# Kernel tuning notes

Hardware: AMD Instinct MI355X
Metric: run time of the kernel (lower is better)

The kernel has to match this reference:

```python
import jax, jax.numpy as jnp
import numpy as np

B = 64; L = 1024; M = 3; PATCH = 16; STRIDE = 8
LEN_S = (L - PATCH) // STRIDE + 2   # patch_num incl. extra patch from replication pad (=128)
LEN_P = 12                           # tokenized prompt length
T = LEN_S + LEN_P                    # total tokens fed to GPT2 (=140)
D = 768; NH = 12; HD = D // NH       # GPT2-small dims
NL = 6; DMLP = 3072                  # gpt_layers, GPT2 MLP width
DFF = 768; NCLS = 10; DLC = 128      # d_ff hidden slice, classes, d_l_comp
SEQ = np.array([1] * LEN_S + [2] * LEN_P)

def _pe(n, d):
    pos = np.arange(n)[:, None].astype(np.float64)
    i = np.arange(0, d, 2)[None, :].astype(np.float64)
    ang = pos / np.power(10000.0, i / d)
    pe = np.zeros((n, d), np.float32)
    pe[:, 0::2] = np.sin(ang); pe[:, 1::2] = np.cos(ang)
    return pe

PE = jnp.asarray(_pe(LEN_S, D))
# allocation matrix (T x 2), column-normalized: maps 2 coarse nodes back to fine tokens
_afc = np.zeros((T, 2), np.float32)
_afc[:LEN_S, 0] = 1.0 / LEN_S; _afc[LEN_S:, 1] = 1.0 / LEN_P
AFC = jnp.asarray(_afc)

def _build_edges():
    # bidirectional chain edges over the token sequence; edge-type 1 = both endpoints are patch tokens
    e, m = [], []
    for i in range(T - 1):
        t = 1 if (SEQ[i] == 1 and SEQ[i + 1] == 1) else 0
        e += [(i, i + 1), (i + 1, i)]; m += [t, t]
    e = np.array(e, np.int32).T            # (2, E0)
    E0 = e.shape[1]
    off = np.arange(B, dtype=np.int32) * T # expand_edges: per-sample node offsets
    ee = (e[:, None, :] + off[None, :, None]).reshape(2, -1)
    mm = np.tile(np.array(m, np.int32), B)
    seg = np.repeat(np.arange(B, dtype=np.int32), E0) * 2 + mm  # (graph, edge-type) segment id
    return ee, seg

def layer_norm(x, g, b, eps=1e-5):
    mu = x.mean(-1, keepdims=True)
    v = ((x - mu) ** 2).mean(-1, keepdims=True)
    return (x - mu) * jax.lax.rsqrt(v + eps) * g + b

def _fwd(x_enc, conv_w, prompt_emb, wpe, ln1_g, ln1_b, attn_w, attn_b, proj_w, proj_b,
         ln2_g, ln2_b, fc1_w, fc1_b, fc2_w, fc2_b, lnf_g, lnf_b,
         ll1_w, ll1_b, ll0_w, ll0_b, l2s_w, l2s_b, w_l2s,
         lnp_g, lnp_b, out_w, out_b, edge_index, edge_seg):
    Bb = x_enc.shape[0]
    # ---- patching (ReplicationPad1d + unfold + 'b m n p -> b n (p m)') ----
    xt = jnp.transpose(x_enc, (0, 2, 1))                                   # (B,M,L)
    xt = jnp.concatenate([xt, jnp.repeat(xt[:, :, -1:], STRIDE, axis=-1)], axis=-1)
    idx = np.arange(LEN_S)[:, None] * STRIDE + np.arange(PATCH)[None, :]
    patches = xt[:, :, idx]                                                # (B,M,N,P)
    inp = jnp.transpose(patches, (0, 2, 3, 1)).reshape(Bb, LEN_S, PATCH * M)
    # ---- DataEmbedding: circular conv1d token embedding + sinusoid pos ----
    xc = jnp.transpose(inp, (0, 2, 1))
    xc = jnp.concatenate([xc[:, :, -1:], xc, xc[:, :, :1]], axis=-1)       # circular pad k=3
    val = jax.lax.conv_general_dilated(xc, conv_w, (1,), 'VALID',
                                       dimension_numbers=('NCH', 'OIH', 'NCH'))
    enc = jnp.transpose(val, (0, 2, 1)) + PE                               # (B,LEN_S,D)
    h0 = jnp.concatenate([enc, jnp.broadcast_to(prompt_emb, (Bb, LEN_P, D))], axis=1)
    # ---- edge weights: cosine similarity + per-(graph,edge-type) softmax norm ----
    src, dst = edge_index[0], edge_index[1]
    flat = h0.reshape(Bb * T, D)
    fs, fd = flat[src], flat[dst]
    cos = jnp.sum(fs * fd, -1) / (jnp.linalg.norm(fs, axis=-1) * jnp.linalg.norm(fd, axis=-1) + 1e-8)
    nseg = 2 * Bb
    mx = jax.ops.segment_max(cos, edge_seg, num_segments=nseg)
    ex = jnp.exp(cos - mx[edge_seg])
    ew = ex / (jax.ops.segment_sum(ex, edge_seg, num_segments=nseg)[edge_seg] + 1e-8)
    # ---- coarse (large) node embeddings via large_layer1/0 on detached features ----
    o1 = jax.lax.stop_gradient(h0[:, :LEN_S]).reshape(Bb, LEN_S * D)
    o2 = jax.lax.stop_gradient(h0[:, LEN_S:]).reshape(Bb, LEN_P * D)
    l_h = jnp.stack([o1 @ ll1_w + ll1_b, o2 @ ll0_w + ll0_b], axis=1)      # (B,2,D)
    # ---- GPT2-with-GNN blocks ----
    h = h0 + wpe[:T]
    causal = np.tril(np.ones((T, T), dtype=bool))
    scale = 1.0 / np.sqrt(HD)
    for l in range(NL):
        x = layer_norm(h, ln1_g[l], ln1_b[l])
        qkv = x @ attn_w[l] + attn_b[l]
        q, k, v = [t.reshape(Bb, T, NH, HD) for t in jnp.split(qkv, 3, axis=-1)]
        s = jnp.einsum('bqhd,bkhd->bhqk', q, k) * scale
        s = jnp.where(causal, s, jnp.finfo(s.dtype).min)
        a = jax.nn.softmax(s, axis=-1)
        o = jnp.einsum('bhqk,bkhd->bqhd', a, v).reshape(Bb, T, D)
        h = h + o @ proj_w[l] + proj_b[l]
        # edge-weighted message passing fused after attention (irregular gather/scatter)
        hf = h.reshape(Bb * T, D)
        agg = jax.ops.segment_sum(ew[:, None] * hf[src], dst, num_segments=Bb * T)
        h = h + agg.reshape(Bb, T, D)
        # MLP (GPT2 gelu_new ~ tanh approx)
        x2 = layer_norm(h, ln2_g[l], ln2_b[l])
        h = h + (jax.nn.gelu(x2 @ fc1_w[l] + fc1_b[l], approximate=True) @ fc2_w[l] + fc2_b[l])
        # coarse 2-node complete graph message passing + large->small fusion via afc/l2s
        l_h = l_h + l_h[:, ::-1, :]
        h = h + w_l2s * jnp.einsum('tl,bld->btd', AFC, l_h[:, :, :DLC] @ l2s_w + l2s_b)
    h = layer_norm(h, lnf_g, lnf_b)
    # ---- classification head: slice d_ff, gelu, flatten, layernorm, linear ----
    z = jax.nn.gelu(h[:, :, :DFF], approximate=False).reshape(Bb, -1)
    z = layer_norm(z, lnp_g, lnp_b)
    return z @ out_w + out_b

def setup_inputs():
    key = jax.random.key(0)
    ks = iter(jax.random.split(key, 40))
    r = lambda *s: jax.random.normal(next(ks), s, jnp.float32) * 0.02
    ee, seg = _build_edges()
    return dict(
        x_enc=jax.random.normal(next(ks), (B, L, M), jnp.float32),
        x_mark_enc=jax.random.normal(next(ks), (B, L, 4), jnp.float32),
        conv_w=r(D, PATCH * M, 3),
        prompt_emb=r(1, LEN_P, D),
        wpe=r(1024, D),
        ln1_g=jnp.ones((NL, D)), ln1_b=jnp.zeros((NL, D)),
        attn_w=r(NL, D, 3 * D), attn_b=jnp.zeros((NL, 3 * D)),
        proj_w=r(NL, D, D), proj_b=jnp.zeros((NL, D)),
        ln2_g=jnp.ones((NL, D)), ln2_b=jnp.zeros((NL, D)),
        fc1_w=r(NL, D, DMLP), fc1_b=jnp.zeros((NL, DMLP)),
        fc2_w=r(NL, DMLP, D), fc2_b=jnp.zeros((NL, D)),
        lnf_g=jnp.ones((D,)), lnf_b=jnp.zeros((D,)),
        ll1_w=r(LEN_S * D, D), ll1_b=jnp.zeros((D,)),
        ll0_w=r(LEN_P * D, D), ll0_b=jnp.zeros((D,)),
        l2s_w=r(DLC, D), l2s_b=jnp.zeros((D,)),
        w_l2s=jnp.float32(0.5),
        lnp_g=jnp.ones((DFF * T,)), lnp_b=jnp.zeros((DFF * T,)),
        out_w=r(DFF * T, NCLS), out_b=jnp.zeros((NCLS,)),
        edge_index=jnp.asarray(ee), edge_seg=jnp.asarray(seg),
    )

def reference(x_enc, x_mark_enc, conv_w, prompt_emb, wpe, ln1_g, ln1_b, attn_w, attn_b,
              proj_w, proj_b, ln2_g, ln2_b, fc1_w, fc1_b, fc2_w, fc2_b, lnf_g, lnf_b,
              ll1_w, ll1_b, ll0_w, ll0_b, l2s_w, l2s_b, w_l2s, lnp_g, lnp_b,
              out_w, out_b, edge_index, edge_seg):
    # x_mark_enc is accepted (matching the torch forward signature) but unused
    return _fwd(x_enc, conv_w, prompt_emb, wpe, ln1_g, ln1_b, attn_w, attn_b, proj_w, proj_b,
                ln2_g, ln2_b, fc1_w, fc1_b, fc2_w, fc2_b, lnf_g, lnf_b,
                ll1_w, ll1_b, ll0_w, ll0_b, l2s_w, l2s_b, w_l2s,
                lnp_g, lnp_b, out_w, out_b, edge_index, edge_seg)
```

## Files before the change

kernel.cpp:

```cpp
#include <hip/hip_runtime.h>
#include <math.h>

#define Bz     64
#define LENS   128
#define LENP   12
#define Tz     140
#define Dz     768
#define NHz    12
#define HDz    64
#define NLz    6
#define DMLPz  3072
#define NCLSz  10
#define EPBz   278
#define NTOKz  (Bz*Tz)
#define ZDIMz  (Tz*Dz)
#define KBIGz  (LENS*Dz)
#define KSMALLz (LENP*Dz)
#define PSTR   168

typedef float f32x4 __attribute__((ext_vector_type(4)));
typedef unsigned int u32x4 __attribute__((ext_vector_type(4)));
typedef short short8 __attribute__((ext_vector_type(8)));

__device__ __forceinline__ float wave_sum(float v){
  #pragma unroll
  for (int m = 32; m; m >>= 1) v += __shfl_xor(v, m);
  return v;
}
__device__ __forceinline__ float wave_max(float v){
  #pragma unroll
  for (int m = 32; m; m >>= 1) v = fmaxf(v, __shfl_xor(v, m));
  return v;
}
__device__ __forceinline__ float red16_max(float v){
  v = fmaxf(v, __shfl_xor(v, 1));
  v = fmaxf(v, __shfl_xor(v, 2));
  v = fmaxf(v, __shfl_xor(v, 4));
  v = fmaxf(v, __shfl_xor(v, 8));
  return v;
}
__device__ __forceinline__ float red16_sum(float v){
  v += __shfl_xor(v, 1); v += __shfl_xor(v, 2);
  v += __shfl_xor(v, 4); v += __shfl_xor(v, 8);
  return v;
}
__device__ __forceinline__ float gelu_tanh(float u){
  float c = 0.7978845608028654f * (u + 0.044715f * u * u * u);
  return 0.5f * u * (1.0f + tanhf(c));
}
__device__ __forceinline__ float gelu_exact(float u){
  return 0.5f * u * (1.0f + erff(u * 0.7071067811865476f));
}

__device__ __forceinline__ unsigned int f2bf(float x){
  unsigned int u = __float_as_uint(x);
  return (u + 0x7fffu + ((u >> 16) & 1u)) >> 16;
}
__device__ __forceinline__ float bf2f(unsigned int h){
  return __uint_as_float(h << 16);
}

__device__ __forceinline__ f32x4 mfma_bf16(u32x4 a, u32x4 b, f32x4 c){
  asm("v_mfma_f32_16x16x32_bf16 %0, %1, %2, %0" : "+v"(c) : "v"(a), "v"(b));
  return c;
}

__device__ __forceinline__ short8 pun(u32x4 u){
  union { u32x4 u; short8 s; } x; x.u = u; return x.s;
}
__device__ __forceinline__ f32x4 mfma_b(u32x4 a, u32x4 b, f32x4 c){
  return __builtin_amdgcn_mfma_f32_16x16x32_bf16(pun(a), pun(b), c, 0, 0, 0);
}

__device__ __forceinline__ void cvt_hilo(f32x4 x0, f32x4 x1, u32x4& h, u32x4& l){
  unsigned int h0 = f2bf(x0[0]), h1 = f2bf(x0[1]), h2 = f2bf(x0[2]), h3 = f2bf(x0[3]);
  unsigned int h4 = f2bf(x1[0]), h5 = f2bf(x1[1]), h6 = f2bf(x1[2]), h7 = f2bf(x1[3]);
  unsigned int l0 = f2bf(x0[0] - bf2f(h0)), l1 = f2bf(x0[1] - bf2f(h1));
  unsigned int l2 = f2bf(x0[2] - bf2f(h2)), l3 = f2bf(x0[3] - bf2f(h3));
  unsigned int l4 = f2bf(x1[0] - bf2f(h4)), l5 = f2bf(x1[1] - bf2f(h5));
  unsigned int l6 = f2bf(x1[2] - bf2f(h6)), l7 = f2bf(x1[3] - bf2f(h7));
  h[0] = h0 | (h1 << 16); h[1] = h2 | (h3 << 16);
  h[2] = h4 | (h5 << 16); h[3] = h6 | (h7 << 16);
  l[0] = l0 | (l1 << 16); l[1] = l2 | (l3 << 16);
  l[2] = l4 | (l5 << 16); l[3] = l6 | (l7 << 16);
}

__global__ void k_pe(float* pe){
  int idx = blockIdx.x * 256 + threadIdx.x;
  int s = idx / Dz, o = idx % Dz;
  int ie = o & ~1;
  double ang = (double)s * pow(10000.0, -(double)ie / (double)Dz);
  pe[idx] = (o & 1) ? (float)cos(ang) : (float)sin(ang);
}

__global__ void k_cwt(const float* __restrict__ cw, float* __restrict__ cwt){
  int idx = blockIdx.x * 256 + threadIdx.x;
  int o = idx % Dz, j = idx / Dz;
  int i = j % 48, k = j / 48;
  cwt[j * Dz + o] = cw[o * 144 + i * 3 + k];
}

__global__ __launch_bounds__(256) void k_conv(const float* __restrict__ x_enc,
                                              const float* __restrict__ cwt,
                                              const float* __restrict__ pe,
                                              float* __restrict__ h0){
  int b = blockIdx.x / LENS, s = blockIdx.x % LENS;
  int tid = threadIdx.x;
  __shared__ float in144[144];
  if (tid < 144){
    int k = tid / 48, i = tid % 48;
    int sp = (s + k - 1 + LENS) % LENS;
    int p = i / 3, m = i % 3;
    int j = sp * 8 + p; if (j > 1023) j = 1023;
    in144[tid] = x_enc[(b * 1024 + j) * 3 + m];
  }
  __syncthreads();
  for (int o = tid; o < Dz; o += 256){
    float acc = pe[s * Dz + o];
    #pragma unroll 8
    for (int j = 0; j < 144; ++j) acc += in144[j] * cwt[j * Dz + o];
    h0[((size_t)(b * Tz + s)) * Dz + o] = acc;
  }
}

__global__ void k_prompt(const float* __restrict__ pr, float* __restrict__ h0){
  int idx = blockIdx.x * 256 + threadIdx.x;
  int b = idx / (LENP * Dz), r = idx % (LENP * Dz);
  h0[((size_t)(b * Tz + LENS)) * Dz + r] = pr[r];
}

__global__ void k_norms(const float* __restrict__ h0, float* __restrict__ nrm){
  int n = blockIdx.x, lane = threadIdx.x;
  const float* r = h0 + (size_t)n * Dz;
  float s = 0.f;
  for (int d = lane; d < Dz; d += 64){ float v = r[d]; s += v * v; }
  s = wave_sum(s);
  if (lane == 0) nrm[n] = sqrtf(s);
}

__global__ void k_ecos(const float* __restrict__ h0, const int* __restrict__ eidx,
                       const float* __restrict__ nrm, float* __restrict__ cosb){
  int e = blockIdx.x, lane = threadIdx.x;
  int sN = eidx[e], dN = eidx[Bz * EPBz + e];
  const float* a = h0 + (size_t)sN * Dz;
  const float* b = h0 + (size_t)dN * Dz;
  float s = 0.f;
  for (int d = lane; d < Dz; d += 64) s += a[d] * b[d];
  s = wave_sum(s);
  if (lane == 0) cosb[e] = s / (nrm[sN] * nrm[dN] + 1e-8f);
}

__global__ __launch_bounds__(256) void k_esoft(const float* __restrict__ cosb,
                                               const int* __restrict__ eseg,
                                               float* __restrict__ ew){
  int b = blockIdx.x, tid = threadIdx.x;
  __shared__ float c[EPBz];
  __shared__ unsigned char gg[EPBz];
  __shared__ float r0[256], r1[256];
  for (int e = tid; e < EPBz; e += 256){
    c[e] = cosb[b * EPBz + e];
    gg[e] = (unsigned char)(eseg[b * EPBz + e] - 2 * b);
  }
  __syncthreads();
  float m0 = -1e30f, m1 = -1e30f;
  for (int e = tid; e < EPBz; e += 256){
    if (gg[e]) m1 = fmaxf(m1, c[e]); else m0 = fmaxf(m0, c[e]);
  }
  r0[tid] = m0; r1[tid] = m1; __syncthreads();
  for (int s = 128; s; s >>= 1){
    if (tid < s){ r0[tid] = fmaxf(r0[tid], r0[tid+s]); r1[tid] = fmaxf(r1[tid], r1[tid+s]); }
    __syncthreads();
  }
  m0 = r0[0]; m1 = r1[0]; __syncthreads();
  float s0 = 0.f, s1 = 0.f;
  for (int e = tid; e < EPBz; e += 256){
    float ex = expf(c[e] - (gg[e] ? m1 : m0));
    c[e] = ex;
    if (gg[e]) s1 += ex; else s0 += ex;
  }
  r0[tid] = s0; r1[tid] = s1; __syncthreads();
  for (int s = 128; s; s >>= 1){
    if (tid < s){ r0[tid] += r0[tid+s]; r1[tid] += r1[tid+s]; }
    __syncthreads();
  }
  s0 = r0[0]; s1 = r1[0];
  for (int e = tid; e < EPBz; e += 256)
    ew[b * EPBz + e] = c[e] / ((gg[e] ? s1 : s0) + 1e-8f);
}

__global__ void k_fills(const float* __restrict__ b1, const float* __restrict__ b0,
                        float* __restrict__ sbuf){
  int idx = blockIdx.x * 256 + threadIdx.x;
  int d = idx % Dz;
  sbuf[idx] = b1[d] + b0[d];
}

__global__ __launch_bounds__(256) void k_splitk(const float* __restrict__ Abase, int aOff,
                                                const float* __restrict__ W,
                                                float* __restrict__ Cacc,
                                                int K, int kChunk){
  __shared__ __align__(16) float As[16 * 65];
  __shared__ __align__(16) float Ws[16 * 64];
  int tid = threadIdx.x, tx = tid % 16, ty = tid / 16;
  int n0 = blockIdx.x * 64;
  int kb = blockIdx.y * kChunk;
  int ke = kb + kChunk; if (ke > K) ke = K;
  float acc[16];
  #pragma unroll
  for (int i = 0; i < 16; ++i) acc[i] = 0.f;
  for (int kk = kb; kk < ke; kk += 16){
    #pragma unroll
    for (int r = 0; r < 4; ++r){
      int idx = tid + r * 256; int k = idx & 15, m = idx >> 4;
      As[k * 65 + m] = Abase[(size_t)m * ZDIMz + aOff + kk + k];
    }
    #pragma unroll
    for (int r = 0; r < 4; ++r){
      int idx = tid + r * 256; int n = idx & 63, k = idx >> 6;
      Ws[k * 64 + n] = W[(size_t)(kk + k) * Dz + n0 + n];
    }
    __syncthreads();
    #pragma unroll
    for (int k = 0; k < 16; ++k){
      float a[4], bvv[4];
      #pragma unroll
      for (int i = 0; i < 4; ++i) a[i] = As[k * 65 + ty * 4 + i];
      #pragma unroll
      for (int j = 0; j < 4; ++j) bvv[j] = Ws[k * 64 + tx * 4 + j];
      #pragma unroll
      for (int i = 0; i < 4; ++i)
        #pragma unroll
        for (int j = 0; j < 4; ++j) acc[i * 4 + j] += a[i] * bvv[j];
    }
    __syncthreads();
  }
  #pragma unroll
  for (int i = 0; i < 4; ++i)
    #pragma unroll
    for (int j = 0; j < 4; ++j)
      atomicAdd(&Cacc[(size_t)(ty * 4 + i) * Dz + n0 + tx * 4 + j], acc[i * 4 + j]);
}

__global__ void k_psmall(const float* __restrict__ sbuf, const float* __restrict__ l2sw,
                         float* __restrict__ P){
  int idx = blockIdx.x * 256 + threadIdx.x;
  int b = idx / Dz, d = idx % Dz;
  float acc = 0.f;
  #pragma unroll 8
  for (int c = 0; c < 128; ++c) acc += sbuf[b * Dz + c] * l2sw[c * Dz + d];
  P[idx] = acc;
}

__global__ void k_addwpe(const float* __restrict__ h0, const float* __restrict__ wpe,
                         float* __restrict__ h){
  size_t idx = (size_t)blockIdx.x * 256 + threadIdx.x;
  int n = (int)(idx / Dz), d = (int)(idx % Dz);
  int t = n % Tz;
  h[idx] = h0[idx] + wpe[t * Dz + d];
}

__global__ __launch_bounds__(256) void k_ln(const float* __restrict__ in, float* __restrict__ out,
                                            const float* __restrict__ g, const float* __restrict__ bb){
  int row = blockIdx.x, tid = threadIdx.x;
  const float* r = in + (size_t)row * Dz;
  float v0 = r[tid], v1 = r[tid + 256], v2 = r[tid + 512];
  __shared__ float red[256];
  red[tid] = v0 + v1 + v2; __syncthreads();
  for (int s = 128; s; s >>= 1){ if (tid < s) red[tid] += red[tid + s]; __syncthreads(); }
  float mu = red[0] * (1.0f / Dz); __syncthreads();
  float d0 = v0 - mu, d1 = v1 - mu, d2 = v2 - mu;
  red[tid] = d0 * d0 + d1 * d1 + d2 * d2; __syncthreads();
  for (int s = 128; s; s >>= 1){ if (tid < s) red[tid] += red[tid + s]; __syncthreads(); }
  float rstd = rsqrtf(red[0] * (1.0f / Dz) + 1e-5f);
  float* o = out + (size_t)row * Dz;
  o[tid]       = d0 * rstd * g[tid]       + bb[tid];
  o[tid + 256] = d1 * rstd * g[tid + 256] + bb[tid + 256];
  o[tid + 512] = d2 * rstd * g[tid + 512] + bb[tid + 512];
}

__global__ __launch_bounds__(256) void k_wt(const float* __restrict__ W,
                                            unsigned short* __restrict__ WT,
                                            int K, int N){
  __shared__ float T[64][65];
  int k0 = blockIdx.y * 64, n0v = blockIdx.x * 64;
  int tid = threadIdx.x;
  int tx = tid & 15, ty = tid >> 4;
  #pragma unroll
  for (int rr = 0; rr < 4; ++rr){
    int row = rr * 16 + ty;
    const float* src = &W[(size_t)(k0 + row) * N + n0v + tx * 4];
    f32x4 v = *(const f32x4*)src;
    T[row][tx * 4]     = v[0];
    T[row][tx * 4 + 1] = v[1];
    T[row][tx * 4 + 2] = v[2];
    T[row][tx * 4 + 3] = v[3];
  }
  __syncthreads();
  #pragma unroll
  for (int s = 0; s < 2; ++s){
    int gi = tid + s * 256;
    int n = gi >> 3, kg = gi & 7;
    unsigned int h[8], l[8];
    #pragma unroll
    for (int j = 0; j < 8; ++j){
      float x = T[kg * 8 + j][n];
      h[j] = f2bf(x);
      l[j] = f2bf(x - bf2f(h[j]));
    }
    u32x4 hv, lv;
    hv[0] = h[0] | (h[1] << 16); hv[1] = h[2] | (h[3] << 16);
    hv[2] = h[4] | (h[5] << 16); hv[3] = h[6] | (h[7] << 16);
    lv[0] = l[0] | (l[1] << 16); lv[1] = l[2] | (l[3] << 16);
    lv[2] = l[4] | (l[5] << 16); lv[3] = l[6] | (l[7] << 16);
    size_t base = (size_t)(n0v + n) * 2 * K + (size_t)(k0 / 8 + kg) * 16;
    *(u32x4*)&WT[base]     = hv;
    *(u32x4*)&WT[base + 8] = lv;
  }
}

template<int MODE>
__global__ __launch_bounds__(256, 2) void k_bgemm(const float* __restrict__ A,
                                                  const unsigned short* __restrict__ WT,
                                                  const float* __restrict__ bias,
                                                  const float* __restrict__ R,
                                                  float* __restrict__ C, int M, int N, int K,
                                                  const float* __restrict__ P,
                                                  const float* __restrict__ l2sb,
                                                  const float* __restrict__ wl2s, float lscale){
  __shared__ __align__(16) unsigned short As[128 * 64];
  __shared__ __align__(16) unsigned short Bs[128 * 64];
  int tid = threadIdx.x;
  int n0 = blockIdx.x * 128, m0 = blockIdx.y * 128;
  int w = tid >> 6, lane = tid & 63;
  int wr = w >> 1, wc = w & 1;
  int g = lane >> 4, q = lane & 15;

  f32x4 acc[4][4];
  #pragma unroll
  for (int i = 0; i < 4; ++i)
    #pragma unroll
    for (int j = 0; j < 4; ++j) acc[i][j] = (f32x4){0.f, 0.f, 0.f, 0.f};

  for (int kk = 0; kk < K; kk += 32){
    #pragma unroll
    for (int s = 0; s < 2; ++s){
      int gi = tid + s * 256;
      int m = gi >> 2, kb = gi & 3;
      const float* src = A + (size_t)(m0 + m) * K + kk + kb * 8;
      f32x4 x0 = *(const f32x4*)src;
      f32x4 x1 = *(const f32x4*)(src + 4);
      u32x4 hv, lv;
      cvt_hilo(x0, x1, hv, lv);
      int sw = (m & 7) << 3;
      unsigned short* rp = &As[m * 64];
      *(u32x4*)&rp[(kb * 16) ^ sw]     = hv;
      *(u32x4*)&rp[(kb * 16 + 8) ^ sw] = lv;
    }
    #pragma unroll
    for (int s = 0; s < 4; ++s){
      int ci = tid + s * 256;
      int n = ci >> 3, c = ci & 7;
      u32x4 v = *(const u32x4*)&WT[(size_t)(n0 + n) * 2 * K + kk * 2 + c * 8];
      int sw = (n & 7) << 3;
      *(u32x4*)&Bs[n * 64 + ((c * 8) ^ sw)] = v;
    }
    __syncthreads();

    u32x4 aH[4], aL[4], bH[4], bL[4];
    #pragma unroll
    for (int f = 0; f < 4; ++f){
      int row = wr * 64 + f * 16 + q;
      int swa = (row & 7) << 3;
      const unsigned short* rp = &As[row * 64];
      aH[f] = *(const u32x4*)&rp[(g * 16) ^ swa];
      aL[f] = *(const u32x4*)&rp[(g * 16 + 8) ^ swa];
      int col = wc * 64 + f * 16 + q;
      int swb = (col & 7) << 3;
      const unsigned short* cp = &Bs[col * 64];
      bH[f] = *(const u32x4*)&cp[(g * 16) ^ swb];
      bL[f] = *(const u32x4*)&cp[(g * 16 + 8) ^ swb];
    }
    #pragma unroll
    for (int i = 0; i < 4; ++i)
      #pragma unroll
      for (int j = 0; j < 4; ++j){
        acc[i][j] = mfma_bf16(aH[i], bH[j], acc[i][j]);
        acc[i][j] = mfma_bf16(aH[i], bL[j], acc[i][j]);
        acc[i][j] = mfma_bf16(aL[i], bH[j], acc[i][j]);
      }
    __syncthreads();
  }

  float wv = 0.f;
  if (MODE == 3) wv = wl2s[0];
  #pragma unroll
  for (int i = 0; i < 4; ++i){
    #pragma unroll
    for (int r = 0; r < 4; ++r){
      int row = m0 + wr * 64 + i * 16 + g * 4 + r;
      int b = row / Tz, t = row % Tz;
      float ct = (t < LENS) ? (1.0f / LENS) : (1.0f / LENP);
      #pragma unroll
      for (int j = 0; j < 4; ++j){
        int col = n0 + wc * 64 + j * 16 + q;
        size_t idx = (size_t)row * N + col;
        float v = acc[i][j][r] + bias[col];
        if (MODE == 1) v += R[idx];
        if (MODE == 2) v = gelu_tanh(v);
        if (MODE == 3){
          v += R[idx];
          v += wv * ct * (lscale * P[b * Dz + col] + l2sb[col]);
        }
        C[idx] = v;
      }
    }
  }
}

__global__ __launch_bounds__(512, 1) void k_attn2(const float* __restrict__ qkv,
                                                  float* __restrict__ obuf){
  int bh = blockIdx.x; int b = bh / NHz, hh = bh % NHz;
  int tid = threadIdx.x, w = tid >> 6, lane = tid & 63;
  int g = lane >> 4, q = lane & 15;

  __shared__ __align__(16) unsigned short Vb[64 * PSTR];
  __shared__ __align__(16) unsigned short Pp[8][16 * PSTR];

  const float* base = qkv + (size_t)b * Tz * (3 * Dz) + hh * HDz;

  for (int e = tid; e < 64 * 160; e += 512){
    int d = e / 160, j = e - d * 160;
    float v = (j < Tz) ? base[(size_t)j * (3 * Dz) + 2 * Dz + d] : 0.f;
    Vb[d * PSTR + j] = (unsigned short)f2bf(v);
  }
  __syncthreads();

  unsigned short* Pw = &Pp[w][0];

  for (int tile = w; tile < 9; tile += 8){
    int i0 = tile * 16;

    u32x4 qh[2], ql[2];
    {
      int row = i0 + q; if (row > Tz - 1) row = Tz - 1;
      const float* qp = base + (size_t)row * (3 * Dz);
      #pragma unroll
      for (int kt = 0; kt < 2; ++kt){
        f32x4 x0 = *(const f32x4*)(qp + kt * 32 + g * 8);
        f32x4 x1 = *(const f32x4*)(qp + kt * 32 + g * 8 + 4);
        cvt_hilo(x0, x1, qh[kt], ql[kt]);
      }
    }

    f32x4 acc[9];
    #pragma unroll
    for (int j = 0; j < 9; ++j) acc[j] = (f32x4){0.f, 0.f, 0.f, 0.f};
    #pragma unroll
    for (int j = 0; j < 9; ++j){
      if (j > tile) continue;
      int col = j * 16 + q; if (col > Tz - 1) col = Tz - 1;
      const float* kp = base + (size_t)col * (3 * Dz) + Dz;
      #pragma unroll
      for (int kt = 0; kt < 2; ++kt){
        f32x4 x0 = *(const f32x4*)(kp + kt * 32 + g * 8);
        f32x4 x1 = *(const f32x4*)(kp + kt * 32 + g * 8 + 4);
        u32x4 kh, kl;
        cvt_hilo(x0, x1, kh, kl);
        acc[j] = mfma_b(qh[kt], kh, acc[j]);
        acc[j] = mfma_b(qh[kt], kl, acc[j]);
        acc[j] = mfma_b(ql[kt], kh, acc[j]);
      }
    }

    #pragma unroll
    for (int r = 0; r < 4; ++r){
      int t = i0 + g * 4 + r;
      float mx = -1e30f;
      #pragma unroll
      for (int j = 0; j < 9; ++j){
        if (j > tile) continue;
        int col = j * 16 + q;
        float s = acc[j][r] * 0.125f;
        bool valid = (col <= t) && (col < Tz);
        s = valid ? s : -1e30f;
        acc[j][r] = s;
        mx = fmaxf(mx, s);
      }
      mx = red16_max(mx);
      float sum = 0.f;
      #pragma unroll
      for (int j = 0; j < 9; ++j){
        if (j > tile) continue;
        float e = expf(acc[j][r] - mx);
        acc[j][r] = e;
        sum += e;
      }
      sum = red16_sum(sum);
      float inv = 1.0f / sum;
      #pragma unroll
      for (int j = 0; j < 9; ++j){
        if (j > tile) continue;
        acc[j][r] *= inv;
      }
    }

    #pragma unroll
    for (int j = 0; j < 10; ++j){
      const int jc = (j < 9) ? j : 0;
      #pragma unroll
      for (int r = 0; r < 4; ++r){
        float p = (j < 9 && j <= tile) ? acc[jc][r] : 0.f;
        Pw[(g * 4 + r) * PSTR + j * 16 + q] = (unsigned short)f2bf(p);
      }
    }
    __builtin_amdgcn_sched_barrier(0);
    asm volatile("s_waitcnt lgkmcnt(0)" ::: "memory");
    __builtin_amdgcn_sched_barrier(0);

    f32x4 oacc[4];
    #pragma unroll
    for (int dt = 0; dt < 4; ++dt) oacc[dt] = (f32x4){0.f, 0.f, 0.f, 0.f};
    #pragma unroll
    for (int kt = 0; kt < 5; ++kt){
      if (kt > (tile >> 1)) continue;
      u32x4 pa = *(const u32x4*)&Pw[q * PSTR + kt * 32 + g * 8];
      #pragma unroll
      for (int dt = 0; dt < 4; ++dt){
        u32x4 vv = *(const u32x4*)&Vb[(dt * 16 + q) * PSTR + kt * 32 + g * 8];
        oacc[dt] = mfma_b(pa, vv, oacc[dt]);
      }
    }

    #pragma unroll
    for (int r = 0; r < 4; ++r){
      int t = i0 + g * 4 + r;
      if (t < Tz){
        float* op = obuf + (size_t)(b * Tz + t) * Dz + hh * HDz;
        #pragma unroll
        for (int dt = 0; dt < 4; ++dt) op[dt * 16 + q] = oacc[dt][r];
      }
    }
  }
}

__global__ void k_gnn(const float* __restrict__ h2, const float* __restrict__ ew,
                      float* __restrict__ h){
  size_t idx = (size_t)blockIdx.x * 256 + threadIdx.x;
  int n = (int)(idx / Dz);
  int b = n / Tz, t = n % Tz;
  float v = h2[idx];
  if (t >= 1)      v += ew[b * EPBz + 2 * (t - 1)]     * h2[idx - Dz];
  if (t <= Tz - 2) v += ew[b * EPBz + 2 * t + 1]       * h2[idx + Dz];
  h[idx] = v;
}

__global__ __launch_bounds__(256) void k_lnfgelu(const float* __restrict__ in, float* __restrict__ out,
                                                 const float* __restrict__ g, const float* __restrict__ bb){
  int row = blockIdx.x, tid = threadIdx.x;
  const float* r = in + (size_t)row * Dz;
  float v0 = r[tid], v1 = r[tid + 256], v2 = r[tid + 512];
  __shared__ float red[256];
  red[tid] = v0 + v1 + v2; __syncthreads();
  for (int s = 128; s; s >>= 1){ if (tid < s) red[tid] += red[tid + s]; __syncthreads(); }
  float mu = red[0] * (1.0f / Dz); __syncthreads();
  float d0 = v0 - mu, d1 = v1 - mu, d2 = v2 - mu;
  red[tid] = d0 * d0 + d1 * d1 + d2 * d2; __syncthreads();
  for (int s = 128; s; s >>= 1){ if (tid < s) red[tid] += red[tid + s]; __syncthreads(); }
  float rstd = rsqrtf(red[0] * (1.0f / Dz) + 1e-5f);
  float* o = out + (size_t)row * Dz;
  o[tid]       = gelu_exact(d0 * rstd * g[tid]       + bb[tid]);
  o[tid + 256] = gelu_exact(d1 * rstd * g[tid + 256] + bb[tid + 256]);
  o[tid + 512] = gelu_exact(d2 * rstd * g[tid + 512] + bb[tid + 512]);
}

__global__ __launch_bounds__(256) void k_zstats(const float* __restrict__ z, float* __restrict__ stat){
  int b = blockIdx.x, tid = threadIdx.x;
  const float* zr = z + (size_t)b * ZDIMz;
  double s = 0.0, qq = 0.0;
  for (int k = tid; k < ZDIMz; k += 256){ double v = zr[k]; s += v; qq += v * v; }
  __shared__ double rs_[256], rq_[256];
  rs_[tid] = s; rq_[tid] = qq; __syncthreads();
  for (int st = 128; st; st >>= 1){
    if (tid < st){ rs_[tid] += rs_[tid + st]; rq_[tid] += rq_[tid + st]; }
    __syncthreads();
  }
  if (tid == 0){
    double mu = rs_[0] / ZDIMz;
    double var = rq_[0] / ZDIMz - mu * mu;
    stat[b] = (float)mu;
    stat[64 + b] = (float)(1.0 / sqrt(var + 1e-5));
  }
}

__global__ __launch_bounds__(256) void k_head(const float* __restrict__ z, const float* __restrict__ stat,
                                              const float* __restrict__ lg, const float* __restrict__ lb,
                                              const float* __restrict__ W, const float* __restrict__ ob,
                                              float* __restrict__ out){
  int b = blockIdx.x, tid = threadIdx.x;
  float mu = stat[b], rs = stat[64 + b];
  const float* zr = z + (size_t)b * ZDIMz;
  float acc[NCLSz];
  #pragma unroll
  for (int j = 0; j < NCLSz; ++j) acc[j] = 0.f;
  for (int k = tid; k < ZDIMz; k += 256){
    float v = (zr[k] - mu) * rs * lg[k] + lb[k];
    const float* wr = W + (size_t)k * NCLSz;
    #pragma unroll
    for (int j = 0; j < NCLSz; ++j) acc[j] += v * wr[j];
  }
  __shared__ float red[256];
  for (int j = 0; j < NCLSz; ++j){
    red[tid] = acc[j]; __syncthreads();
    for (int s = 128; s; s >>= 1){ if (tid < s) red[tid] += red[tid + s]; __syncthreads(); }
    if (tid == 0) out[b * NCLSz + j] = red[0] + ob[j];
    __syncthreads();
  }
}

extern "C" void kernel_launch(void* const* d_in, const int* in_sizes, int n_in,
                              void* d_out, int out_size, void* d_ws, size_t ws_size,
                              hipStream_t stream){
  const float* x_enc  = (const float*)d_in[0];
  const float* conv_w = (const float*)d_in[2];
  const float* prompt = (const float*)d_in[3];
  const float* wpe    = (const float*)d_in[4];
  const float* ln1_g  = (const float*)d_in[5];
  const float* ln1_b  = (const float*)d_in[6];
  const float* attn_w = (const float*)d_in[7];
  const float* attn_b = (const float*)d_in[8];
  const float* proj_w = (const float*)d_in[9];
  const float* proj_b = (const float*)d_in[10];
  const float* ln2_g  = (const float*)d_in[11];
  const float* ln2_b  = (const float*)d_in[12];
  const float* fc1_w  = (const float*)d_in[13];
  const float* fc1_b  = (const float*)d_in[14];
  const float* fc2_w  = (const float*)d_in[15];
  const float* fc2_b  = (const float*)d_in[16];
  const float* lnf_g  = (const float*)d_in[17];
  const float* lnf_b  = (const float*)d_in[18];
  const float* ll1_w  = (const float*)d_in[19];
  const float* ll1_b  = (const float*)d_in[20];
  const float* ll0_w  = (const float*)d_in[21];
  const float* ll0_b  = (const float*)d_in[22];
  const float* l2s_w  = (const float*)d_in[23];
  const float* l2s_b  = (const float*)d_in[24];
  const float* w_l2s  = (const float*)d_in[25];
  const float* lnp_g  = (const float*)d_in[26];
  const float* lnp_b  = (const float*)d_in[27];
  const float* out_w  = (const float*)d_in[28];
  const float* out_b  = (const float*)d_in[29];
  const int*   eidx   = (const int*)d_in[30];
  const int*   eseg   = (const int*)d_in[31];
  float* out = (float*)d_out;

  float* ws = (float*)d_ws;
  const size_t SZ_H = (size_t)NTOKz * Dz;
  float* h0   = ws;
  float* hbuf = ws + SZ_H;
  float* xb   = ws + 2 * SZ_H;
  float* h2   = ws + 3 * SZ_H;
  float* qkv  = ws + 4 * SZ_H;
  float* big  = qkv + (size_t)NTOKz * 3 * Dz;
  float* pe   = big + (size_t)NTOKz * DMLPz;
  float* cwt  = pe + (size_t)LENS * Dz;
  float* sbuf = cwt + 144 * Dz;
  float* Pbuf = sbuf + Bz * Dz;
  float* nrm  = Pbuf + Bz * Dz;
  float* cosb = nrm + NTOKz;
  float* ewb  = cosb + Bz * EPBz;
  float* stat = ewb + Bz * EPBz;
  unsigned short* WT = (unsigned short*)(stat + 128);

  k_pe    <<<(LENS * Dz) / 256, 256, 0, stream>>>(pe);
  k_cwt   <<<(144 * Dz) / 256, 256, 0, stream>>>(conv_w, cwt);
  k_conv  <<<Bz * LENS, 256, 0, stream>>>(x_enc, cwt, pe, h0);
  k_prompt<<<(Bz * LENP * Dz) / 256, 256, 0, stream>>>(prompt, h0);
  k_norms <<<NTOKz, 64, 0, stream>>>(h0, nrm);
  k_ecos  <<<Bz * EPBz, 64, 0, stream>>>(h0, eidx, nrm, cosb);
  k_esoft <<<Bz, 256, 0, stream>>>(cosb, eseg, ewb);
  k_fills <<<(Bz * Dz) / 256, 256, 0, stream>>>(ll1_b, ll0_b, sbuf);
  k_splitk<<<dim3(Dz / 64, 96), 256, 0, stream>>>(h0, 0,     ll1_w, sbuf, KBIGz,  1024);
  k_splitk<<<dim3(Dz / 64, 9),  256, 0, stream>>>(h0, KBIGz, ll0_w, sbuf, KSMALLz, 1024);
  k_psmall<<<(Bz * Dz) / 256, 256, 0, stream>>>(sbuf, l2s_w, Pbuf);
  k_addwpe<<<(int)(SZ_H / 256), 256, 0, stream>>>(h0, wpe, hbuf);

  for (int l = 0; l < NLz; ++l){
    k_ln<<<NTOKz, 256, 0, stream>>>(hbuf, xb, ln1_g + l * Dz, ln1_b + l * Dz);

    k_wt<<<dim3(3 * Dz / 64, Dz / 64), 256, 0, stream>>>(
        attn_w + (size_t)l * Dz * 3 * Dz, WT, Dz, 3 * Dz);
    k_bgemm<0><<<dim3(3 * Dz / 128, NTOKz / 128), 256, 0, stream>>>(
        xb, WT, attn_b + l * 3 * Dz, nullptr, qkv,
        NTOKz, 3 * Dz, Dz, nullptr, nullptr, nullptr, 0.f);

    k_attn2<<<Bz * NHz, 512, 0, stream>>>(qkv, xb);

    k_wt<<<dim3(Dz / 64, Dz / 64), 256, 0, stream>>>(
        proj_w + (size_t)l * Dz * Dz, WT, Dz, Dz);
    k_bgemm<1><<<dim3(Dz / 128, NTOKz / 128), 256, 0, stream>>>(
        xb, WT, proj_b + l * Dz, hbuf, h2,
        NTOKz, Dz, Dz, nullptr, nullptr, nullptr, 0.f);

    k_gnn<<<(int)(SZ_H / 256), 256, 0, stream>>>(h2, ewb, hbuf);
    k_ln<<<NTOKz, 256, 0, stream>>>(hbuf, xb, ln2_g + l * Dz, ln2_b + l * Dz);

    k_wt<<<dim3(DMLPz / 64, Dz / 64), 256, 0, stream>>>(
        fc1_w + (size_t)l * Dz * DMLPz, WT, Dz, DMLPz);
    k_bgemm<2><<<dim3(DMLPz / 128, NTOKz / 128), 256, 0, stream>>>(
        xb, WT, fc1_b + l * DMLPz, nullptr, big,
        NTOKz, DMLPz, Dz, nullptr, nullptr, nullptr, 0.f);

    k_wt<<<dim3(Dz / 64, DMLPz / 64), 256, 0, stream>>>(
        fc2_w + (size_t)l * DMLPz * Dz, WT, DMLPz, Dz);
    k_bgemm<3><<<dim3(Dz / 128, NTOKz / 128), 256, 0, stream>>>(
        big, WT, fc2_b + l * Dz, hbuf, hbuf,
        NTOKz, Dz, DMLPz, Pbuf, l2s_b, w_l2s, (float)(1 << l));
  }

  k_lnfgelu<<<NTOKz, 256, 0, stream>>>(hbuf, xb, lnf_g, lnf_b);
  k_zstats <<<Bz, 256, 0, stream>>>(xb, stat);
  k_head   <<<Bz, 256, 0, stream>>>(xb, stat, lnp_g, lnp_b, out_w, out_b, out);
}
```

Before: 4.856 ms.

## Pre-split activations to swizzled bf16 hi/lo and stream GEMM tiles via global_load_lds

```diff
diff --git a/kernel.cpp b/kernel.cpp
--- a/kernel.cpp
+++ b/kernel.cpp
@@ -27,11 +27,6 @@
   for (int m = 32; m; m >>= 1) v += __shfl_xor(v, m);
   return v;
 }
-__device__ __forceinline__ float wave_max(float v){
-  #pragma unroll
-  for (int m = 32; m; m >>= 1) v = fmaxf(v, __shfl_xor(v, m));
-  return v;
-}
 __device__ __forceinline__ float red16_max(float v){
   v = fmaxf(v, __shfl_xor(v, 1));
   v = fmaxf(v, __shfl_xor(v, 2));
@@ -64,12 +59,17 @@
   asm("v_mfma_f32_16x16x32_bf16 %0, %1, %2, %0" : "+v"(c) : "v"(a), "v"(b));
   return c;
 }
-
 __device__ __forceinline__ short8 pun(u32x4 u){
   union { u32x4 u; short8 s; } x; x.u = u; return x.s;
 }
 __device__ __forceinline__ f32x4 mfma_b(u32x4 a, u32x4 b, f32x4 c){
   return __builtin_amdgcn_mfma_f32_16x16x32_bf16(pun(a), pun(b), c, 0, 0, 0);
+}
+
+__device__ __forceinline__ void gl_lds16(const void* g, void* l){
+  __builtin_amdgcn_global_load_lds(
+      (const __attribute__((address_space(1))) unsigned int*)g,
+      (__attribute__((address_space(3))) unsigned int*)l, 16, 0, 0);
 }
 
 __device__ __forceinline__ void cvt_hilo(f32x4 x0, f32x4 x1, u32x4& h, u32x4& l){
@@ -83,6 +83,10 @@
   h[2] = h4 | (h5 << 16); h[3] = h6 | (h7 << 16);
   l[0] = l0 | (l1 << 16); l[1] = l2 | (l3 << 16);
   l[2] = l4 | (l5 << 16); l[3] = l6 | (l7 << 16);
+}
+
+__device__ __forceinline__ int swz_chunk(int C, int r){
+  return (C & ~7) | ((C & 7) ^ (r & 7));
 }
 
 __global__ void k_pe(float* pe){
@@ -208,18 +212,21 @@
   float acc[16];
   #pragma unroll
   for (int i = 0; i < 16; ++i) acc[i] = 0.f;
+  int mA = tid >> 2, kqA = (tid & 3) * 4;
+  int nB = (tid * 4) & 63, kB = tid >> 4;
+  f32x4 ra = *(const f32x4*)&Abase[(size_t)mA * ZDIMz + aOff + kb + kqA];
+  f32x4 rw = *(const f32x4*)&W[(size_t)(kb + kB) * Dz + n0 + nB];
   for (int kk = kb; kk < ke; kk += 16){
-    #pragma unroll
-    for (int r = 0; r < 4; ++r){
-      int idx = tid + r * 256; int k = idx & 15, m = idx >> 4;
-      As[k * 65 + m] = Abase[(size_t)m * ZDIMz + aOff + kk + k];
-    }
-    #pragma unroll
-    for (int r = 0; r < 4; ++r){
-      int idx = tid + r * 256; int n = idx & 63, k = idx >> 6;
-      Ws[k * 64 + n] = W[(size_t)(kk + k) * Dz + n0 + n];
-    }
+    As[(kqA + 0) * 65 + mA] = ra[0];
+    As[(kqA + 1) * 65 + mA] = ra[1];
+    As[(kqA + 2) * 65 + mA] = ra[2];
+    As[(kqA + 3) * 65 + mA] = ra[3];
+    *(f32x4*)&Ws[kB * 64 + nB] = rw;
     __syncthreads();
+    if (kk + 16 < ke){
+      ra = *(const f32x4*)&Abase[(size_t)mA * ZDIMz + aOff + kk + 16 + kqA];
+      rw = *(const f32x4*)&W[(size_t)(kk + 16 + kB) * Dz + n0 + nB];
+    }
     #pragma unroll
     for (int k = 0; k < 16; ++k){
       float a[4], bvv[4];
@@ -259,12 +266,16 @@
   h[idx] = h0[idx] + wpe[t * Dz + d];
 }
 
-__global__ __launch_bounds__(256) void k_ln(const float* __restrict__ in, float* __restrict__ out,
-                                            const float* __restrict__ g, const float* __restrict__ bb){
+__global__ __launch_bounds__(256) void k_lnx(const float* __restrict__ in,
+                                             unsigned short* __restrict__ XA,
+                                             const float* __restrict__ g,
+                                             const float* __restrict__ bb){
   int row = blockIdx.x, tid = threadIdx.x;
   const float* r = in + (size_t)row * Dz;
+  __shared__ float buf[768];
+  __shared__ float red[256];
   float v0 = r[tid], v1 = r[tid + 256], v2 = r[tid + 512];
-  __shared__ float red[256];
+  buf[tid] = v0; buf[tid + 256] = v1; buf[tid + 512] = v2;
   red[tid] = v0 + v1 + v2; __syncthreads();
   for (int s = 128; s; s >>= 1){ if (tid < s) red[tid] += red[tid + s]; __syncthreads(); }
   float mu = red[0] * (1.0f / Dz); __syncthreads();
@@ -272,10 +283,21 @@
   red[tid] = d0 * d0 + d1 * d1 + d2 * d2; __syncthreads();
   for (int s = 128; s; s >>= 1){ if (tid < s) red[tid] += red[tid + s]; __syncthreads(); }
   float rstd = rsqrtf(red[0] * (1.0f / Dz) + 1e-5f);
-  float* o = out + (size_t)row * Dz;
-  o[tid]       = d0 * rstd * g[tid]       + bb[tid];
-  o[tid + 256] = d1 * rstd * g[tid + 256] + bb[tid + 256];
-  o[tid + 512] = d2 * rstd * g[tid + 512] + bb[tid + 512];
+  if (tid < 96){
+    int kg = tid;
+    f32x4 g0 = *(const f32x4*)&g[kg * 8],  g1 = *(const f32x4*)&g[kg * 8 + 4];
+    f32x4 b0 = *(const f32x4*)&bb[kg * 8], b1 = *(const f32x4*)&bb[kg * 8 + 4];
+    f32x4 x0, x1;
+    #pragma unroll
+    for (int j = 0; j < 4; ++j) x0[j] = (buf[kg * 8 + j]     - mu) * rstd * g0[j] + b0[j];
+    #pragma unroll
+    for (int j = 0; j < 4; ++j) x1[j] = (buf[kg * 8 + 4 + j] - mu) * rstd * g1[j] + b1[j];
+    u32x4 hv, lv;
+    cvt_hilo(x0, x1, hv, lv);
+    size_t rb = (size_t)row * 1536;
+    *(u32x4*)&XA[rb + swz_chunk(kg * 2,     row) * 8] = hv;
+    *(u32x4*)&XA[rb + swz_chunk(kg * 2 + 1, row) * 8] = lv;
+  }
 }
 
 __global__ __launch_bounds__(256) void k_wt(const float* __restrict__ W,
@@ -312,14 +334,17 @@
     hv[2] = h[4] | (h[5] << 16); hv[3] = h[6] | (h[7] << 16);
     lv[0] = l[0] | (l[1] << 16); lv[1] = l[2] | (l[3] << 16);
     lv[2] = l[4] | (l[5] << 16); lv[3] = l[6] | (l[7] << 16);
-    size_t base = (size_t)(n0v + n) * 2 * K + (size_t)(k0 / 8 + kg) * 16;
-    *(u32x4*)&WT[base]     = hv;
-    *(u32x4*)&WT[base + 8] = lv;
-  }
-}
-
-template<int MODE>
+    int r = n0v + n;
+    int C0 = (k0 / 8 + kg) * 2;
+    size_t rb = (size_t)r * 2 * K;
+    *(u32x4*)&WT[rb + swz_chunk(C0,     r) * 8] = hv;
+    *(u32x4*)&WT[rb + swz_chunk(C0 + 1, r) * 8] = lv;
+  }
+}
+
+template<int MODE, int AFMT>
 __global__ __launch_bounds__(256, 2) void k_bgemm(const float* __restrict__ A,
+                                                  const unsigned short* __restrict__ AX,
                                                   const unsigned short* __restrict__ WT,
                                                   const float* __restrict__ bias,
                                                   const float* __restrict__ R,
@@ -341,28 +366,39 @@
     #pragma unroll
     for (int j = 0; j < 4; ++j) acc[i][j] = (f32x4){0.f, 0.f, 0.f, 0.f};
 
+  const size_t rbytes = (size_t)K * 4;
+
   for (int kk = 0; kk < K; kk += 32){
-    #pragma unroll
-    for (int s = 0; s < 2; ++s){
-      int gi = tid + s * 256;
-      int m = gi >> 2, kb = gi & 3;
-      const float* src = A + (size_t)(m0 + m) * K + kk + kb * 8;
-      f32x4 x0 = *(const f32x4*)src;
-      f32x4 x1 = *(const f32x4*)(src + 4);
-      u32x4 hv, lv;
-      cvt_hilo(x0, x1, hv, lv);
-      int sw = (m & 7) << 3;
-      unsigned short* rp = &As[m * 64];
-      *(u32x4*)&rp[(kb * 16) ^ sw]     = hv;
-      *(u32x4*)&rp[(kb * 16 + 8) ^ sw] = lv;
+    if (AFMT == 1){
+      #pragma unroll
+      for (int s = 0; s < 4; ++s){
+        int i16 = tid + s * 256;
+        int m = i16 >> 3, cc = i16 & 7;
+        const char* src = (const char*)AX + (size_t)(m0 + m) * rbytes + (size_t)kk * 4 + cc * 16;
+        gl_lds16(src, (char*)As + (size_t)i16 * 16);
+      }
+    } else {
+      #pragma unroll
+      for (int s = 0; s < 2; ++s){
+        int gi = tid + s * 256;
+        int m = gi >> 2, kb2 = gi & 3;
+        const float* src = A + (size_t)(m0 + m) * K + kk + kb2 * 8;
+        f32x4 x0 = *(const f32x4*)src;
+        f32x4 x1 = *(const f32x4*)(src + 4);
+        u32x4 hv, lv;
+        cvt_hilo(x0, x1, hv, lv);
+        int sw = (m & 7) << 3;
+        unsigned short* rp = &As[m * 64];
+        *(u32x4*)&rp[(kb2 * 16) ^ sw]     = hv;
+        *(u32x4*)&rp[(kb2 * 16 + 8) ^ sw] = lv;
+      }
     }
     #pragma unroll
     for (int s = 0; s < 4; ++s){
-      int ci = tid + s * 256;
-      int n = ci >> 3, c = ci & 7;
-      u32x4 v = *(const u32x4*)&WT[(size_t)(n0 + n) * 2 * K + kk * 2 + c * 8];
-      int sw = (n & 7) << 3;
-      *(u32x4*)&Bs[n * 64 + ((c * 8) ^ sw)] = v;
+      int i16 = tid + s * 256;
+      int n = i16 >> 3, cc = i16 & 7;
+      const char* src = (const char*)WT + (size_t)(n0 + n) * rbytes + (size_t)kk * 4 + cc * 16;
+      gl_lds16(src, (char*)Bs + (size_t)i16 * 16);
     }
     __syncthreads();
 
@@ -418,7 +454,7 @@
 }
 
 __global__ __launch_bounds__(512, 1) void k_attn2(const float* __restrict__ qkv,
-                                                  float* __restrict__ obuf){
+                                                  unsigned short* __restrict__ XA){
   int bh = blockIdx.x; int b = bh / NHz, hh = bh % NHz;
   int tid = threadIdx.x, w = tid >> 6, lane = tid & 63;
   int g = lane >> 4, q = lane & 15;
@@ -531,15 +567,41 @@
       }
     }
 
-    #pragma unroll
-    for (int r = 0; r < 4; ++r){
-      int t = i0 + g * 4 + r;
+    float* Pf = (float*)Pw;
+    __builtin_amdgcn_sched_barrier(0);
+    asm volatile("s_waitcnt lgkmcnt(0)" ::: "memory");
+    __builtin_amdgcn_sched_barrier(0);
+    #pragma unroll
+    for (int r = 0; r < 4; ++r)
+      #pragma unroll
+      for (int dt = 0; dt < 4; ++dt)
+        Pf[(g * 4 + r) * 64 + dt * 16 + q] = oacc[dt][r];
+    __builtin_amdgcn_sched_barrier(0);
+    asm volatile("s_waitcnt lgkmcnt(0)" ::: "memory");
+    __builtin_amdgcn_sched_barrier(0);
+    #pragma unroll
+    for (int s = 0; s < 2; ++s){
+      int gi = lane + s * 64;
+      int r16 = gi >> 3, kg8 = gi & 7;
+      int t = i0 + r16;
       if (t < Tz){
-        float* op = obuf + (size_t)(b * Tz + t) * Dz + hh * HDz;
+        int m = b * Tz + t;
+        f32x4 x0, x1;
         #pragma unroll
-        for (int dt = 0; dt < 4; ++dt) op[dt * 16 + q] = oacc[dt][r];
-      }
-    }
+        for (int j = 0; j < 4; ++j) x0[j] = Pf[r16 * 64 + kg8 * 8 + j];
+        #pragma unroll
+        for (int j = 0; j < 4; ++j) x1[j] = Pf[r16 * 64 + kg8 * 8 + 4 + j];
+        u32x4 hv, lv;
+        cvt_hilo(x0, x1, hv, lv);
+        int C0 = (hh * 8 + kg8) * 2;
+        size_t rb = (size_t)m * 1536;
+        *(u32x4*)&XA[rb + swz_chunk(C0,     m) * 8] = hv;
+        *(u32x4*)&XA[rb + swz_chunk(C0 + 1, m) * 8] = lv;
+      }
+    }
+    __builtin_amdgcn_sched_barrier(0);
+    asm volatile("s_waitcnt lgkmcnt(0)" ::: "memory");
+    __builtin_amdgcn_sched_barrier(0);
   }
 }
 
@@ -670,6 +732,7 @@
   float* ewb  = cosb + Bz * EPBz;
   float* stat = ewb + Bz * EPBz;
   unsigned short* WT = (unsigned short*)(stat + 128);
+  unsigned short* XA = (unsigned short*)xb;
 
   k_pe    <<<(LENS * Dz) / 256, 256, 0, stream>>>(pe);
   k_cwt   <<<(144 * Dz) / 256, 256, 0, stream>>>(conv_w, cwt);
@@ -679,41 +742,41 @@
   k_ecos  <<<Bz * EPBz, 64, 0, stream>>>(h0, eidx, nrm, cosb);
   k_esoft <<<Bz, 256, 0, stream>>>(cosb, eseg, ewb);
   k_fills <<<(Bz * Dz) / 256, 256, 0, stream>>>(ll1_b, ll0_b, sbuf);
-  k_splitk<<<dim3(Dz / 64, 96), 256, 0, stream>>>(h0, 0,     ll1_w, sbuf, KBIGz,  1024);
-  k_splitk<<<dim3(Dz / 64, 9),  256, 0, stream>>>(h0, KBIGz, ll0_w, sbuf, KSMALLz, 1024);
+  k_splitk<<<dim3(Dz / 64, KBIGz / 512), 256, 0, stream>>>(h0, 0,     ll1_w, sbuf, KBIGz,  512);
+  k_splitk<<<dim3(Dz / 64, KSMALLz / 512), 256, 0, stream>>>(h0, KBIGz, ll0_w, sbuf, KSMALLz, 512);
   k_psmall<<<(Bz * Dz) / 256, 256, 0, stream>>>(sbuf, l2s_w, Pbuf);
   k_addwpe<<<(int)(SZ_H / 256), 256, 0, stream>>>(h0, wpe, hbuf);
 
   for (int l = 0; l < NLz; ++l){
-    k_ln<<<NTOKz, 256, 0, stream>>>(hbuf, xb, ln1_g + l * Dz, ln1_b + l * Dz);
+    k_lnx<<<NTOKz, 256, 0, stream>>>(hbuf, XA, ln1_g + l * Dz, ln1_b + l * Dz);
 
     k_wt<<<dim3(3 * Dz / 64, Dz / 64), 256, 0, stream>>>(
         attn_w + (size_t)l * Dz * 3 * Dz, WT, Dz, 3 * Dz);
-    k_bgemm<0><<<dim3(3 * Dz / 128, NTOKz / 128), 256, 0, stream>>>(
-        xb, WT, attn_b + l * 3 * Dz, nullptr, qkv,
+    k_bgemm<0, 1><<<dim3(3 * Dz / 128, NTOKz / 128), 256, 0, stream>>>(
+        nullptr, XA, WT, attn_b + l * 3 * Dz, nullptr, qkv,
         NTOKz, 3 * Dz, Dz, nullptr, nullptr, nullptr, 0.f);
 
-    k_attn2<<<Bz * NHz, 512, 0, stream>>>(qkv, xb);
+    k_attn2<<<Bz * NHz, 512, 0, stream>>>(qkv, XA);
 
     k_wt<<<dim3(Dz / 64, Dz / 64), 256, 0, stream>>>(
         proj_w + (size_t)l * Dz * Dz, WT, Dz, Dz);
-    k_bgemm<1><<<dim3(Dz / 128, NTOKz / 128), 256, 0, stream>>>(
-        xb, WT, proj_b + l * Dz, hbuf, h2,
+    k_bgemm<1, 1><<<dim3(Dz / 128, NTOKz / 128), 256, 0, stream>>>(
+        nullptr, XA, WT, proj_b + l * Dz, hbuf, h2,
         NTOKz, Dz, Dz, nullptr, nullptr, nullptr, 0.f);
 
     k_gnn<<<(int)(SZ_H / 256), 256, 0, stream>>>(h2, ewb, hbuf);
-    k_ln<<<NTOKz, 256, 0, stream>>>(hbuf, xb, ln2_g + l * Dz, ln2_b + l * Dz);
+    k_lnx<<<NTOKz, 256, 0, stream>>>(hbuf, XA, ln2_g + l * Dz, ln2_b + l * Dz);
 
     k_wt<<<dim3(DMLPz / 64, Dz / 64), 256, 0, stream>>>(
         fc1_w + (size_t)l * Dz * DMLPz, WT, Dz, DMLPz);
-    k_bgemm<2><<<dim3(DMLPz / 128, NTOKz / 128), 256, 0, stream>>>(
-        xb, WT, fc1_b + l * DMLPz, nullptr, big,
+    k_bgemm<2, 1><<<dim3(DMLPz / 128, NTOKz / 128), 256, 0, stream>>>(
+        nullptr, XA, WT, fc1_b + l * DMLPz, nullptr, big,
         NTOKz, DMLPz, Dz, nullptr, nullptr, nullptr, 0.f);
 
     k_wt<<<dim3(Dz / 64, DMLPz / 64), 256, 0, stream>>>(
         fc2_w + (size_t)l * DMLPz * Dz, WT, DMLPz, Dz);
-    k_bgemm<3><<<dim3(Dz / 128, NTOKz / 128), 256, 0, stream>>>(
-        big, WT, fc2_b + l * Dz, hbuf, hbuf,
+    k_bgemm<3, 0><<<dim3(Dz / 128, NTOKz / 128), 256, 0, stream>>>(
+        big, nullptr, WT, fc2_b + l * Dz, hbuf, hbuf,
         NTOKz, Dz, DMLPz, Pbuf, l2s_b, w_l2s, (float)(1 << l));
   }
 
```

After: 4.725 ms. -2.7%, faster.
